# Performance work log

Measured on AMD Instinct MI355X. Metric: run time of the kernel, lower is better.

The kernel has to match this reference:

```python
import jax, jax.numpy as jnp
import numpy as np


def setup_inputs() -> dict:
    key = jax.random.key(0)
    k1, k2, k3, k4 = jax.random.split(key, 4)
    N, E, F_IN, H, C = 100000, 1600000, 128, 64, 64
    x = jax.random.normal(k1, (N, F_IN), dtype=jnp.float32)
    edge_index = jax.random.randint(k2, (2, E), 0, N, dtype=jnp.int64)
    W1 = jax.random.normal(k3, (F_IN, H), dtype=jnp.float32) / np.sqrt(F_IN)
    b1 = jnp.zeros((H,), dtype=jnp.float32)
    W2 = jax.random.normal(k4, (H, C), dtype=jnp.float32) / np.sqrt(H)
    b2 = jnp.zeros((C,), dtype=jnp.float32)
    return {"x": x, "edge_index": edge_index, "W1": W1, "b1": b1, "W2": W2, "b2": b2}


def reference(x, edge_index, W1, b1, W2, b2):
    N = x.shape[0]
    # add self-loops (PyG GCNConv default)
    loop = jnp.arange(N, dtype=edge_index.dtype)
    src = jnp.concatenate([edge_index[0], loop])
    dst = jnp.concatenate([edge_index[1], loop])
    # symmetric normalization: deg^{-1/2}[src] * deg^{-1/2}[dst], deg over dst
    deg = jax.ops.segment_sum(jnp.ones_like(dst, dtype=x.dtype), dst, num_segments=N)
    dis = jnp.where(deg > 0, jax.lax.rsqrt(deg), 0.0)
    norm = dis[src] * dis[dst]  # [E+N]

    def gcn_conv(h, W, b):
        h = h @ W                                   # [N, out]
        msg = h[src] * norm[:, None]                # [E+N, out] gather
        agg = jax.ops.segment_sum(msg, dst, num_segments=N)  # scatter-add
        return agg + b

    h = jax.nn.relu(gcn_conv(x, W1, b1))
    # dropout inactive in eval mode
    out = gcn_conv(h, W2, b2)
    return jax.nn.log_softmax(out, axis=1)
```

## Files before the change

### kernel.cpp

```cpp
#include <hip/hip_runtime.h>
#include <cstdint>
#include <cstddef>

#define PASSA_EDGES 8192
#define PASSB_CAP   12288


__device__ __forceinline__ unsigned short f2bf(float f) {
    unsigned int u = __float_as_uint(f);
    u += 0x7FFFu + ((u >> 16) & 1u);
    return (unsigned short)(u >> 16);
}

__device__ __forceinline__ void bf8_fma(uint4 u, float w, float* acc) {
    acc[0] += __uint_as_float(u.x << 16) * w;
    acc[1] += __uint_as_float(u.x & 0xFFFF0000u) * w;
    acc[2] += __uint_as_float(u.y << 16) * w;
    acc[3] += __uint_as_float(u.y & 0xFFFF0000u) * w;
    acc[4] += __uint_as_float(u.z << 16) * w;
    acc[5] += __uint_as_float(u.z & 0xFFFF0000u) * w;
    acc[6] += __uint_as_float(u.w << 16) * w;
    acc[7] += __uint_as_float(u.w & 0xFFFF0000u) * w;
}
__device__ __forceinline__ void bf8_unpack(uint4 u, float* v) {
    v[0] = __uint_as_float(u.x << 16);
    v[1] = __uint_as_float(u.x & 0xFFFF0000u);
    v[2] = __uint_as_float(u.y << 16);
    v[3] = __uint_as_float(u.y & 0xFFFF0000u);
    v[4] = __uint_as_float(u.z << 16);
    v[5] = __uint_as_float(u.z & 0xFFFF0000u);
    v[6] = __uint_as_float(u.w << 16);
    v[7] = __uint_as_float(u.w & 0xFFFF0000u);
}


__global__ void bcur_init(int* __restrict__ bcur, int NBUCK, int CAP) {
    int b = threadIdx.x;
    if (b < NBUCK) bcur[b] = b * CAP;
}


__global__ __launch_bounds__(256) void passA(const int* __restrict__ src,
                                             const int* __restrict__ dst,
                                             int* __restrict__ bcur,
                                             int2* __restrict__ bbuf, int E,
                                             int CAP, int shift) {
    __shared__ int2 bins[PASSA_EDGES];
    __shared__ int  cnt[256], off[256], cur[256], gbase[256];
    const int t  = threadIdx.x;
    const int e0 = blockIdx.x * PASSA_EDGES;
    const int n  = min(PASSA_EDGES, E - e0);

    cnt[t] = 0;
    __syncthreads();
    for (int i = t; i < n; i += 256) atomicAdd(&cnt[dst[e0 + i] >> shift], 1);
    __syncthreads();

    int v = cnt[t];
    off[t] = v;
    __syncthreads();
    for (int o = 1; o < 256; o <<= 1) {
        int u = (t >= o) ? off[t - o] : 0;
        __syncthreads();
        off[t] += u;
        __syncthreads();
    }
    int excl = off[t] - v;
    off[t]   = excl;
    cur[t]   = excl;
    __syncthreads();

    for (int i = t; i < n; i += 256) {
        int d = dst[e0 + i];
        int s = src[e0 + i];
        int p = atomicAdd(&cur[d >> shift], 1);
        bins[p] = make_int2(s, d);
    }
    if (cnt[t] > 0) gbase[t] = atomicAdd(&bcur[t], cnt[t]);
    __syncthreads();

    const int w = t >> 6, lane = t & 63;
    for (int b = w; b < 256; b += 4) {
        int c = cnt[b];
        if (c == 0) continue;
        int lo  = off[b], go = gbase[b];
        int lim = (b + 1) * CAP;
        if (go + c > lim) c = max(0, lim - go);
        for (int i = lane; i < c; i += 64) bbuf[go + i] = bins[lo + i];
    }
}


__global__ __launch_bounds__(256) void hist_dis(const int2* __restrict__ bbuf,
                                                const int* __restrict__ bcur,
                                                int* __restrict__ hist,
                                                float* __restrict__ dis,
                                                int N, int CAP, int shift) {
    __shared__ int cnt[1024];
    const int b     = blockIdx.x;
    const int node0 = b << shift;
    const int nn    = min(1 << shift, N - node0);
    for (int j = threadIdx.x; j < nn; j += 256) cnt[j] = 0;
    __syncthreads();
    const int start = b * CAP, end = bcur[b];
    for (int e = start + threadIdx.x; e < end; e += 256)
        atomicAdd(&cnt[bbuf[e].y - node0], 1);
    __syncthreads();
    for (int j = threadIdx.x; j < nn; j += 256) {
        int c = cnt[j];
        hist[node0 + j] = (c + 7) & ~7;
        dis[node0 + j]  = rsqrtf((float)(c + 1));
    }
}


__global__ __launch_bounds__(256) void scan_partial(const int* __restrict__ hist,
                                                    int* __restrict__ partials, int N) {
    __shared__ int red[256];
    const int t    = threadIdx.x;
    const int base = blockIdx.x * 1024 + t * 4;
    int s = 0;
    if (base + 3 < N) {
        int4 v = *(const int4*)&hist[base];
        s = v.x + v.y + v.z + v.w;
    } else {
        for (int i = 0; i < 4; i++)
            if (base + i < N) s += hist[base + i];
    }
    red[t] = s;
    __syncthreads();
    for (int off = 128; off; off >>= 1) {
        if (t < off) red[t] += red[t + off];
        __syncthreads();
    }
    if (t == 0) partials[blockIdx.x] = red[0];
}

__global__ __launch_bounds__(256) void scan_offsets(int* __restrict__ partials, int NB) {
    __shared__ int tmp[256];
    const int t = threadIdx.x;
    int v = (t < NB) ? partials[t] : 0;
    tmp[t] = v;
    __syncthreads();
    for (int off = 1; off < 256; off <<= 1) {
        int u = (t >= off) ? tmp[t - off] : 0;
        __syncthreads();
        tmp[t] += u;
        __syncthreads();
    }
    if (t < NB) partials[t] = tmp[t] - v;
}

__global__ __launch_bounds__(256) void scan_apply(const int* __restrict__ hist,
                                                  const int* __restrict__ partials,
                                                  int* __restrict__ ptr, int N) {
    __shared__ int tsum[256];
    const int t    = threadIdx.x;
    const int base = blockIdx.x * 1024 + t * 4;
    int v[4];
    int s = 0;
    for (int i = 0; i < 4; i++) {
        v[i] = (base + i < N) ? hist[base + i] : 0;
        s += v[i];
    }
    tsum[t] = s;
    __syncthreads();
    for (int off = 1; off < 256; off <<= 1) {
        int u = (t >= off) ? tsum[t - off] : 0;
        __syncthreads();
        tsum[t] += u;
        __syncthreads();
    }
    int run = partials[blockIdx.x] + tsum[t] - s;
    for (int i = 0; i < 4; i++) {
        if (base + i < N) {
            ptr[base + i] = run;
            run += v[i];
        }
    }
    if (base <= N - 1 && N - 1 < base + 4) ptr[N] = run;
}


__global__ __launch_bounds__(256) void passB(const int2* __restrict__ bbuf,
                                             const int* __restrict__ bcur,
                                             const int* __restrict__ ptr,
                                             int2* __restrict__ csrw,
                                             const float* __restrict__ dis,
                                             int N, int CAP, int shift) {
    __shared__ int lcnt[1024];
    __shared__ int lcsr[PASSB_CAP];
    const int b     = blockIdx.x;
    const int node0 = b << shift;
    const int nn    = min(1 << shift, N - node0);
    const int cbase = ptr[node0];
    const int csize = ptr[node0 + nn] - cbase;

    for (int j = threadIdx.x; j < nn; j += 256) lcnt[j] = ptr[node0 + j] - cbase;
    __syncthreads();

    const int start = b * CAP, end = bcur[b];
    if (csize <= PASSB_CAP) {
        for (int i = threadIdx.x; i < csize; i += 256) lcsr[i] = -1;
        __syncthreads();
        for (int e = start + threadIdx.x; e < end; e += 256) {
            int2 pr = bbuf[e];
            int  p  = atomicAdd(&lcnt[pr.y - node0], 1);
            lcsr[p] = pr.x;
        }
        __syncthreads();
        for (int i = threadIdx.x; i < csize; i += 256) {
            int s = lcsr[i];
            csrw[cbase + i] = (s < 0) ? make_int2(0, 0)
                                      : make_int2(s, __float_as_int(dis[s]));
        }
    } else {
        for (int i = threadIdx.x; i < csize; i += 256) csrw[cbase + i] = make_int2(0, 0);
        __syncthreads();
        for (int e = start + threadIdx.x; e < end; e += 256) {
            int2 pr = bbuf[e];
            int  p  = atomicAdd(&lcnt[pr.y - node0], 1);
            csrw[cbase + p] = make_int2(pr.x, __float_as_int(dis[pr.x]));
        }
    }
}


template <int K>
__global__ __launch_bounds__(256) void gemm64_bf16(const float* __restrict__ X,
                                                   const float* __restrict__ W,
                                                   unsigned short* __restrict__ Yb, int N) {
    __shared__ float ws[K * 64];
    const int tid  = threadIdx.x;
    const int row0 = blockIdx.x * 64;

    const float4* W4 = (const float4*)W;
    for (int i = tid; i < K * 16; i += 256) ((float4*)ws)[i] = W4[i];

    const int cg = tid & 15;
    const int rg = tid >> 4;

    const float* xr[4];
#pragma unroll
    for (int i = 0; i < 4; i++) {
        int r = row0 + rg * 4 + i;
        xr[i] = X + (size_t)min(r, N - 1) * K;
    }
    __syncthreads();

    float acc[4][4] = {};
#pragma unroll 2
    for (int k = 0; k < K; k += 4) {
        float4 xf[4], wf[4];
#pragma unroll
        for (int i = 0; i < 4; i++) xf[i] = *(const float4*)(xr[i] + k);
#pragma unroll
        for (int j = 0; j < 4; j++) wf[j] = *(const float4*)&ws[(k + j) * 64 + cg * 4];
#pragma unroll
        for (int i = 0; i < 4; i++) {
            float4 xv = xf[i];
            acc[i][0] += xv.x * wf[0].x + xv.y * wf[1].x + xv.z * wf[2].x + xv.w * wf[3].x;
            acc[i][1] += xv.x * wf[0].y + xv.y * wf[1].y + xv.z * wf[2].y + xv.w * wf[3].y;
            acc[i][2] += xv.x * wf[0].z + xv.y * wf[1].z + xv.z * wf[2].z + xv.w * wf[3].z;
            acc[i][3] += xv.x * wf[0].w + xv.y * wf[1].w + xv.z * wf[2].w + xv.w * wf[3].w;
        }
    }

#pragma unroll
    for (int i = 0; i < 4; i++) {
        int r = row0 + rg * 4 + i;
        if (r < N) {
            ushort4 o;
            o.x = f2bf(acc[i][0]); o.y = f2bf(acc[i][1]);
            o.z = f2bf(acc[i][2]); o.w = f2bf(acc[i][3]);
            *(ushort4*)&Yb[(size_t)r * 64 + cg * 4] = o;
        }
    }
}


__device__ __forceinline__ void gather8_pad(const unsigned short* __restrict__ B,
                                            const int2* __restrict__ csrw,
                                            int s0, int iters, int co, float* acc) {
    const int4* cs = (const int4*)(csrw + s0);
    int4 c0 = make_int4(0, 0, 0, 0), c1 = c0, c2 = c0, c3 = c0;
    if (iters > 0) { c0 = cs[0]; c1 = cs[1]; c2 = cs[2]; c3 = cs[3]; }
    for (int it = 0; it < iters; ++it) {
        const int nb = min(it + 1, iters - 1) * 4;
        int4 n0 = cs[nb], n1 = cs[nb + 1], n2 = cs[nb + 2], n3 = cs[nb + 3];
        uint4 u0 = *(const uint4*)&B[(size_t)c0.x * 64 + co * 8];
        uint4 u1 = *(const uint4*)&B[(size_t)c0.z * 64 + co * 8];
        uint4 u2 = *(const uint4*)&B[(size_t)c1.x * 64 + co * 8];
        uint4 u3 = *(const uint4*)&B[(size_t)c1.z * 64 + co * 8];
        uint4 u4 = *(const uint4*)&B[(size_t)c2.x * 64 + co * 8];
        uint4 u5 = *(const uint4*)&B[(size_t)c2.z * 64 + co * 8];
        uint4 u6 = *(const uint4*)&B[(size_t)c3.x * 64 + co * 8];
        uint4 u7 = *(const uint4*)&B[(size_t)c3.z * 64 + co * 8];
        bf8_fma(u0, __int_as_float(c0.y), acc);
        bf8_fma(u1, __int_as_float(c0.w), acc);
        bf8_fma(u2, __int_as_float(c1.y), acc);
        bf8_fma(u3, __int_as_float(c1.w), acc);
        bf8_fma(u4, __int_as_float(c2.y), acc);
        bf8_fma(u5, __int_as_float(c2.w), acc);
        bf8_fma(u6, __int_as_float(c3.y), acc);
        bf8_fma(u7, __int_as_float(c3.w), acc);
        c0 = n0; c1 = n1; c2 = n2; c3 = n3;
    }
}


__global__ __launch_bounds__(256) void agg_l1(const unsigned short* __restrict__ B,
                                              const int2* __restrict__ csrw,
                                              const int* __restrict__ ptr,
                                              const float* __restrict__ dis,
                                              const float* __restrict__ b1,
                                              float* __restrict__ hs, int N) {
    const int wid  = threadIdx.x >> 6;
    const int lane = threadIdx.x & 63;
    const int eg   = lane >> 3;
    const int co   = lane & 7;

    const int  row = blockIdx.x * 32 + wid * 8 + eg;
    const bool hr  = (row < N);

    const int   s0 = hr ? ptr[row] : 0;
    const int   s1 = hr ? ptr[row + 1] : 0;
    const float di = hr ? dis[row] : 0.f;
    const int   iters = (s1 - s0) >> 3;

    float acc[8] = {};
    gather8_pad(B, csrw, s0, iters, co, acc);

    if (!hr) return;

    uint4 us = *(const uint4*)&B[(size_t)row * 64 + co * 8];
    float bs[8];
    bf8_unpack(us, bs);
    float bb[8];
    *(float4*)&bb[0] = *(const float4*)&b1[co * 8];
    *(float4*)&bb[4] = *(const float4*)&b1[co * 8 + 4];

    float h[8];
#pragma unroll
    for (int i = 0; i < 8; i++)
        h[i] = fmaxf((acc[i] + bs[i] * di) * di + bb[i], 0.f);

    *(float4*)&hs[(size_t)row * 64 + co * 8]     = make_float4(h[0], h[1], h[2], h[3]);
    *(float4*)&hs[(size_t)row * 64 + co * 8 + 4] = make_float4(h[4], h[5], h[6], h[7]);
}


__global__ __launch_bounds__(256) void agg_l2(const unsigned short* __restrict__ B,
                                              const int2* __restrict__ csrw,
                                              const int* __restrict__ ptr,
                                              const float* __restrict__ dis,
                                              const float* __restrict__ b2,
                                              float* __restrict__ out, int N) {
    const int wid  = threadIdx.x >> 6;
    const int lane = threadIdx.x & 63;
    const int eg   = lane >> 3;
    const int co   = lane & 7;

    const int  row = blockIdx.x * 32 + wid * 8 + eg;
    const bool hr  = (row < N);

    const int   s0 = hr ? ptr[row] : 0;
    const int   s1 = hr ? ptr[row + 1] : 0;
    const float di = hr ? dis[row] : 0.f;
    const int   iters = (s1 - s0) >> 3;

    float acc[8] = {};
    gather8_pad(B, csrw, s0, iters, co, acc);

    if (!hr) return;

    uint4 us = *(const uint4*)&B[(size_t)row * 64 + co * 8];
    float bs[8];
    bf8_unpack(us, bs);
    float bb[8];
    *(float4*)&bb[0] = *(const float4*)&b2[co * 8];
    *(float4*)&bb[4] = *(const float4*)&b2[co * 8 + 4];

    float v[8];
#pragma unroll
    for (int i = 0; i < 8; i++) v[i] = (acc[i] + bs[i] * di) * di + bb[i];

    float m = v[0];
#pragma unroll
    for (int i = 1; i < 8; i++) m = fmaxf(m, v[i]);
#pragma unroll
    for (int off = 1; off <= 4; off <<= 1) m = fmaxf(m, __shfl_xor(m, off));
    float s = 0.f;
#pragma unroll
    for (int i = 0; i < 8; i++) s += __expf(v[i] - m);
#pragma unroll
    for (int off = 1; off <= 4; off <<= 1) s += __shfl_xor(s, off);
    float lse = m + __logf(s);

    float4 oa = make_float4(v[0] - lse, v[1] - lse, v[2] - lse, v[3] - lse);
    float4 ob = make_float4(v[4] - lse, v[5] - lse, v[6] - lse, v[7] - lse);
    *(float4*)&out[(size_t)row * 64 + co * 8]     = oa;
    *(float4*)&out[(size_t)row * 64 + co * 8 + 4] = ob;
}


extern "C" void kernel_launch(void* const* d_in, const int* in_sizes, int n_in,
                              void* d_out, int out_size, void* d_ws, size_t ws_size,
                              hipStream_t stream) {
    const float* x   = (const float*)d_in[0];
    const int*   ei  = (const int*)d_in[1];
    const float* W1  = (const float*)d_in[2];
    const float* b1  = (const float*)d_in[3];
    const float* W2  = (const float*)d_in[4];
    const float* b2  = (const float*)d_in[5];
    float*       out = (float*)d_out;

    const int  N   = in_sizes[0] / 128;
    const int  E   = in_sizes[1] / 2;
    const int* src = ei;
    const int* dst = ei + E;
    const int  NB  = (N + 1023) / 1024;

    int shift = 9;
    while (((N - 1) >> shift) >= 256) shift++;
    const int NBUCK = ((N - 1) >> shift) + 1;
    const int CAP   = ((E / NBUCK) * 3 / 2 + 255) & ~255;

    auto align256 = [](size_t v) { return (v + 255) & ~(size_t)255; };
    char*           p        = (char*)d_ws;
    float*          dis      = (float*)p;          p += align256((size_t)N * 4);
    int*            ptr      = (int*)p;            p += align256((size_t)(N + 1) * 4);
    int*            hist     = (int*)p;            p += align256((size_t)N * 4);
    int*            partials = (int*)p;            p += align256((size_t)NB * 4);
    int*            bcur     = (int*)p;            p += align256(256 * 4);
    int2*           csrw     = (int2*)p;           p += align256(((size_t)E + 8 * (size_t)N) * 8);
    int2*           bbuf     = (int2*)p;           p += align256((size_t)NBUCK * CAP * 8);
    unsigned short* xwb      = (unsigned short*)p; p += align256((size_t)N * 64 * 2);
    unsigned short* hwb      = (unsigned short*)p; p += align256((size_t)N * 64 * 2);

    float* hs = out;

    bcur_init<<<1, 256, 0, stream>>>(bcur, NBUCK, CAP);
    passA<<<(E + PASSA_EDGES - 1) / PASSA_EDGES, 256, 0, stream>>>(src, dst, bcur, bbuf, E, CAP, shift);
    hist_dis<<<NBUCK, 256, 0, stream>>>(bbuf, bcur, hist, dis, N, CAP, shift);
    scan_partial<<<NB, 256, 0, stream>>>(hist, partials, N);
    scan_offsets<<<1, 256, 0, stream>>>(partials, NB);
    scan_apply<<<NB, 256, 0, stream>>>(hist, partials, ptr, N);
    passB<<<NBUCK, 256, 0, stream>>>(bbuf, bcur, ptr, csrw, dis, N, CAP, shift);

    gemm64_bf16<128><<<(N + 63) / 64, 256, 0, stream>>>(x, W1, xwb, N);
    agg_l1<<<(N + 31) / 32, 256, 0, stream>>>(xwb, csrw, ptr, dis, b1, hs, N);
    gemm64_bf16<64><<<(N + 63) / 64, 256, 0, stream>>>(hs, W2, xwb, N);
    agg_l2<<<(N + 31) / 32, 256, 0, stream>>>(xwb, csrw, ptr, dis, b2, out, N);
}
```

Measured before the change: 288.2 us.

## Use split-bf16 MFMA for the dense feature transforms

Replaces the scalar FP32 GEMM kernels with MFMA bf16 16x16x32 kernels. Weights are pre-split into hi/lo bf16 fragments by a small prep kernel, and activations are split in registers, so three MFMAs per tile keep near-FP32 accuracy. The X tile is staged through padded shared memory. The aim is to cut ALU time in the two GEMMs at the cost of an extra tiny kernel launch and 3x MFMA work.

```diff
diff --git a/kernel.cpp b/kernel.cpp
--- a/kernel.cpp
+++ b/kernel.cpp
@@ -4,12 +4,18 @@
 
 #define PASSA_EDGES 8192
 #define PASSB_CAP   12288
+
+typedef __attribute__((ext_vector_type(8))) short bf16x8;
+typedef __attribute__((ext_vector_type(4))) float f32x4;
 
 
 __device__ __forceinline__ unsigned short f2bf(float f) {
     unsigned int u = __float_as_uint(f);
     u += 0x7FFFu + ((u >> 16) & 1u);
     return (unsigned short)(u >> 16);
+}
+__device__ __forceinline__ float bf2f(unsigned short h) {
+    return __uint_as_float((unsigned int)h << 16);
 }
 
 __device__ __forceinline__ void bf8_fma(uint4 u, float w, float* acc) {
@@ -226,56 +232,87 @@
 }
 
 
+__global__ __launch_bounds__(256) void prep_wfrag(const float* __restrict__ W1,
+                                                  const float* __restrict__ W2,
+                                                  unsigned short* __restrict__ whi1,
+                                                  unsigned short* __restrict__ wlo1,
+                                                  unsigned short* __restrict__ whi2,
+                                                  unsigned short* __restrict__ wlo2) {
+    for (int e = threadIdx.x; e < 128 * 64; e += 256) {
+        const int blk = e >> 9, l = (e >> 3) & 63, j = e & 7;
+        const int k = (blk >> 2) * 32 + (l >> 4) * 8 + j;
+        const int n = (blk & 3) * 16 + (l & 15);
+        const float v = W1[k * 64 + n];
+        const unsigned short h = f2bf(v);
+        whi1[e] = h;
+        wlo1[e] = f2bf(v - bf2f(h));
+    }
+    for (int e = threadIdx.x; e < 64 * 64; e += 256) {
+        const int blk = e >> 9, l = (e >> 3) & 63, j = e & 7;
+        const int k = (blk >> 2) * 32 + (l >> 4) * 8 + j;
+        const int n = (blk & 3) * 16 + (l & 15);
+        const float v = W2[k * 64 + n];
+        const unsigned short h = f2bf(v);
+        whi2[e] = h;
+        wlo2[e] = f2bf(v - bf2f(h));
+    }
+}
+
+
 template <int K>
-__global__ __launch_bounds__(256) void gemm64_bf16(const float* __restrict__ X,
-                                                   const float* __restrict__ W,
-                                                   unsigned short* __restrict__ Yb, int N) {
-    __shared__ float ws[K * 64];
+__global__ __launch_bounds__(256) void gemm_mfma(const float* __restrict__ X,
+                                                 const unsigned short* __restrict__ whi,
+                                                 const unsigned short* __restrict__ wlo,
+                                                 unsigned short* __restrict__ Yb, int N) {
+    constexpr int LDX = K + 4;
+    __shared__ float xs[64 * LDX];
     const int tid  = threadIdx.x;
     const int row0 = blockIdx.x * 64;
 
-    const float4* W4 = (const float4*)W;
-    for (int i = tid; i < K * 16; i += 256) ((float4*)ws)[i] = W4[i];
-
-    const int cg = tid & 15;
-    const int rg = tid >> 4;
-
-    const float* xr[4];
-#pragma unroll
-    for (int i = 0; i < 4; i++) {
-        int r = row0 + rg * 4 + i;
-        xr[i] = X + (size_t)min(r, N - 1) * K;
-    }
-    __syncthreads();
-
-    float acc[4][4] = {};
-#pragma unroll 2
-    for (int k = 0; k < K; k += 4) {
-        float4 xf[4], wf[4];
-#pragma unroll
-        for (int i = 0; i < 4; i++) xf[i] = *(const float4*)(xr[i] + k);
-#pragma unroll
-        for (int j = 0; j < 4; j++) wf[j] = *(const float4*)&ws[(k + j) * 64 + cg * 4];
-#pragma unroll
-        for (int i = 0; i < 4; i++) {
-            float4 xv = xf[i];
-            acc[i][0] += xv.x * wf[0].x + xv.y * wf[1].x + xv.z * wf[2].x + xv.w * wf[3].x;
-            acc[i][1] += xv.x * wf[0].y + xv.y * wf[1].y + xv.z * wf[2].y + xv.w * wf[3].y;
-            acc[i][2] += xv.x * wf[0].z + xv.y * wf[1].z + xv.z * wf[2].z + xv.w * wf[3].z;
-            acc[i][3] += xv.x * wf[0].w + xv.y * wf[1].w + xv.z * wf[2].w + xv.w * wf[3].w;
-        }
-    }
-
-#pragma unroll
-    for (int i = 0; i < 4; i++) {
-        int r = row0 + rg * 4 + i;
-        if (r < N) {
-            ushort4 o;
-            o.x = f2bf(acc[i][0]); o.y = f2bf(acc[i][1]);
-            o.z = f2bf(acc[i][2]); o.w = f2bf(acc[i][3]);
-            *(ushort4*)&Yb[(size_t)r * 64 + cg * 4] = o;
-        }
-    }
+#pragma unroll
+    for (int i = 0; i < (64 * K) / 1024; ++i) {
+        const int fidx = i * 1024 + tid * 4;
+        const int r = fidx / K, c = fidx % K;
+        const float4 v = *(const float4*)(X + (size_t)min(row0 + r, N - 1) * K + c);
+        *(float4*)&xs[r * LDX + c] = v;
+    }
+    __syncthreads();
+
+    const int w = tid >> 6, l = tid & 63;
+    const int m = l & 15, kg = l >> 4;
+
+    f32x4 acc[4] = {};
+    const float* xrow = &xs[(w * 16 + m) * LDX];
+
+#pragma unroll
+    for (int s = 0; s < K / 32; ++s) {
+        const float4 a0 = *(const float4*)(xrow + s * 32 + kg * 8);
+        const float4 a1 = *(const float4*)(xrow + s * 32 + kg * 8 + 4);
+        const float av[8] = {a0.x, a0.y, a0.z, a0.w, a1.x, a1.y, a1.z, a1.w};
+        bf16x8 ahi, alo;
+#pragma unroll
+        for (int j = 0; j < 8; ++j) {
+            const unsigned short h = f2bf(av[j]);
+            ahi[j] = (short)h;
+            alo[j] = (short)f2bf(av[j] - bf2f(h));
+        }
+#pragma unroll
+        for (int nt = 0; nt < 4; ++nt) {
+            const bf16x8 bh = *(const bf16x8*)&whi[(s * 4 + nt) * 512 + l * 8];
+            const bf16x8 bl = *(const bf16x8*)&wlo[(s * 4 + nt) * 512 + l * 8];
+            acc[nt] = __builtin_amdgcn_mfma_f32_16x16x32_bf16(ahi, bh, acc[nt], 0, 0, 0);
+            acc[nt] = __builtin_amdgcn_mfma_f32_16x16x32_bf16(alo, bh, acc[nt], 0, 0, 0);
+            acc[nt] = __builtin_amdgcn_mfma_f32_16x16x32_bf16(ahi, bl, acc[nt], 0, 0, 0);
+        }
+    }
+
+#pragma unroll
+    for (int nt = 0; nt < 4; ++nt)
+#pragma unroll
+        for (int r = 0; r < 4; ++r) {
+            const int row = row0 + w * 16 + kg * 4 + r;
+            if (row < N) Yb[(size_t)row * 64 + nt * 16 + m] = f2bf(acc[nt][r]);
+        }
 }
 
 
@@ -436,11 +473,15 @@
     int2*           csrw     = (int2*)p;           p += align256(((size_t)E + 8 * (size_t)N) * 8);
     int2*           bbuf     = (int2*)p;           p += align256((size_t)NBUCK * CAP * 8);
     unsigned short* xwb      = (unsigned short*)p; p += align256((size_t)N * 64 * 2);
-    unsigned short* hwb      = (unsigned short*)p; p += align256((size_t)N * 64 * 2);
+    unsigned short* whi1     = (unsigned short*)p; p += align256(128 * 64 * 2);
+    unsigned short* wlo1     = (unsigned short*)p; p += align256(128 * 64 * 2);
+    unsigned short* whi2     = (unsigned short*)p; p += align256(64 * 64 * 2);
+    unsigned short* wlo2     = (unsigned short*)p; p += align256(64 * 64 * 2);
 
     float* hs = out;
 
     bcur_init<<<1, 256, 0, stream>>>(bcur, NBUCK, CAP);
+    prep_wfrag<<<1, 256, 0, stream>>>(W1, W2, whi1, wlo1, whi2, wlo2);
     passA<<<(E + PASSA_EDGES - 1) / PASSA_EDGES, 256, 0, stream>>>(src, dst, bcur, bbuf, E, CAP, shift);
     hist_dis<<<NBUCK, 256, 0, stream>>>(bbuf, bcur, hist, dis, N, CAP, shift);
     scan_partial<<<NB, 256, 0, stream>>>(hist, partials, N);
@@ -448,8 +489,8 @@
     scan_apply<<<NB, 256, 0, stream>>>(hist, partials, ptr, N);
     passB<<<NBUCK, 256, 0, stream>>>(bbuf, bcur, ptr, csrw, dis, N, CAP, shift);
 
-    gemm64_bf16<128><<<(N + 63) / 64, 256, 0, stream>>>(x, W1, xwb, N);
+    gemm_mfma<128><<<(N + 63) / 64, 256, 0, stream>>>(x, whi1, wlo1, xwb, N);
     agg_l1<<<(N + 31) / 32, 256, 0, stream>>>(xwb, csrw, ptr, dis, b1, hs, N);
-    gemm64_bf16<64><<<(N + 63) / 64, 256, 0, stream>>>(hs, W2, xwb, N);
+    gemm_mfma<64><<<(N + 63) / 64, 256, 0, stream>>>(hs, whi2, wlo2, xwb, N);
     agg_l2<<<(N + 31) / 32, 256, 0, stream>>>(xwb, csrw, ptr, dis, b2, out, N);
 }
```

Result: faster. 266.9 us (-7.4%).
